# Kernel optimization log

Measured on AMD Instinct MI355X. Metric: run time of the kernel, lower is better.

## Reference

```python
import jax, jax.numpy as jnp
import numpy as np

N_NODES = 100000


def gcn_conv(x, edge_index, W, b, n_nodes):
    # PyG GCNConv: x' = D^{-1/2} (A + I) D^{-1/2} (X W) + b
    xw = x @ W  # [N, out]
    # add self loops
    loops = jnp.arange(n_nodes, dtype=edge_index.dtype)
    row = jnp.concatenate([edge_index[0], loops])  # source
    col = jnp.concatenate([edge_index[1], loops])  # target (aggregation index)
    # symmetric degree normalization based on target degree (with self loops)
    deg = jax.ops.segment_sum(jnp.ones_like(col, dtype=xw.dtype), col,
                              num_segments=n_nodes)
    dinv = jnp.where(deg > 0, jax.lax.rsqrt(deg), 0.0)
    norm = dinv[row] * dinv[col]  # [E+N]
    msgs = norm[:, None] * xw[row]  # [E+N, out]
    out = jax.ops.segment_sum(msgs, col, num_segments=n_nodes)
    return out + b


def setup_inputs() -> dict:
    key = jax.random.key(0)
    k1, k2, k3, k4 = jax.random.split(key, 4)
    N, F_in, H, C, E = N_NODES, 128, 16, 10, 3200000
    x = jax.random.normal(k1, (N, F_in), dtype=jnp.float32)
    edge_index = jax.random.randint(k2, (2, E), 0, N, dtype=jnp.int64)
    W1 = jax.random.normal(k3, (F_in, H), dtype=jnp.float32) / np.sqrt(F_in)
    b1 = jnp.zeros((H,), dtype=jnp.float32)
    W2 = jax.random.normal(k4, (H, C), dtype=jnp.float32) / np.sqrt(H)
    b2 = jnp.zeros((C,), dtype=jnp.float32)
    return {"x": x, "edge_index": edge_index, "W1": W1, "b1": b1,
            "W2": W2, "b2": b2}


def reference(x, edge_index, W1, b1, W2, b2):
    n = x.shape[0]
    h = jax.nn.relu(gcn_conv(x, edge_index, W1, b1, n))
    # dropout is identity in eval mode
    logits = gcn_conv(h, edge_index, W2, b2, n)
    return jax.nn.log_softmax(logits, axis=1)
```

## Files before the change

kernel.cpp:

```cpp
#include <hip/hip_runtime.h>
#include <hip/hip_bf16.h>
#include <math.h>

#define F_IN 128
#define HID  16
#define NCLS 10
#define BS   256
#define CH   16384
#define KPL  4

typedef unsigned int uint;
typedef unsigned short ushort;
typedef __attribute__((ext_vector_type(8))) short short8v;
typedef __attribute__((ext_vector_type(4))) float f32x4;

static __device__ __forceinline__ short f2bf(float f) {
    __hip_bfloat16 h = __float2bfloat16(f);
    return *reinterpret_cast<short*>(&h);
}
static __device__ __forceinline__ float bflo(uint u) {
    union { uint x; float f; } c; c.x = u << 16; return c.f;
}
static __device__ __forceinline__ float bfhi(uint u) {
    union { uint x; float f; } c; c.x = u & 0xffff0000u; return c.f;
}
static __device__ __forceinline__ uint packbf(float f0, float f1) {
    return (uint)(ushort)f2bf(f0) | ((uint)(ushort)f2bf(f1) << 16);
}

__global__ __launch_bounds__(1024) void k_hist2(const int* __restrict__ col, int* __restrict__ hist,
                                                int E, int nbv, int nchunk) {
    extern __shared__ int h[];
    int t = threadIdx.x, k = blockIdx.x;
    for (int i = t; i < nbv; i += 1024) h[i] = 0;
    __syncthreads();
    int start = k * CH, end = min(start + CH, E);
    for (int i = start + t; i < end; i += 1024) atomicAdd(&h[col[i] >> 8], 1);
    __syncthreads();
    for (int i = t; i < nbv; i += 1024) hist[(size_t)i * nchunk + k] = h[i];
}

__global__ void k_cscan(int* __restrict__ hist, int* __restrict__ bcnt, int nchunk, int nbv) {
    int wave = threadIdx.x >> 6, lane = threadIdx.x & 63;
    int b = blockIdx.x * 4 + wave;
    if (b >= nbv) return;
    int* hb = hist + (size_t)b * nchunk;
    int vals[KPL];
    int ls = 0;
    #pragma unroll
    for (int i = 0; i < KPL; ++i) {
        int k = lane * KPL + i;
        vals[i] = (k < nchunk) ? hb[k] : 0;
        ls += vals[i];
    }
    int inc = ls;
    #pragma unroll
    for (int d = 1; d < 64; d <<= 1) {
        int v = __shfl_up(inc, d, 64);
        if (lane >= d) inc += v;
    }
    int run = inc - ls;
    #pragma unroll
    for (int i = 0; i < KPL; ++i) {
        int k = lane * KPL + i;
        if (k < nchunk) { hb[k] = run; run += vals[i]; }
    }
    if (lane == 63) bcnt[b] = inc;
}

__global__ void k_bscan(const int* __restrict__ bcnt, int* __restrict__ boff, int nbv, int E) {
    __shared__ int s[512];
    int t = threadIdx.x;
    int v = (t < nbv) ? bcnt[t] : 0;
    s[t] = v;
    __syncthreads();
    for (int ofs = 1; ofs < 512; ofs <<= 1) {
        int val = (t >= ofs) ? s[t - ofs] : 0;
        __syncthreads();
        if (t >= ofs) s[t] += val;
        __syncthreads();
    }
    if (t < nbv) boff[t] = s[t] - v;
    if (t == nbv) boff[t] = E;
}

__global__ __launch_bounds__(1024) void k_binW(const int* __restrict__ row, const int* __restrict__ col,
                                               const int* __restrict__ hist, const int* __restrict__ boff,
                                               uint* __restrict__ pairs, int E, int nbv, int nchunk) {
    extern __shared__ int lds[];
    int* gbase = lds;
    int* cur   = lds + nbv;
    int t = threadIdx.x, k = blockIdx.x;
    for (int i = t; i < nbv; i += 1024) {
        gbase[i] = boff[i] + hist[(size_t)i * nchunk + k];
        cur[i] = 0;
    }
    __syncthreads();
    int start = k * CH, end = min(start + CH, E);
    for (int i = start + t; i < end; i += 1024) {
        int c = col[i];
        int b = c >> 8;
        int rk = atomicAdd(&cur[b], 1);
        pairs[gbase[b] + rk] = ((uint)row[i] << 8) | (uint)(c & (BS - 1));
    }
}

__global__ __launch_bounds__(1024) void k_nsp(const uint* __restrict__ pairs,
                                              const int* __restrict__ boff,
                                              int* __restrict__ off, float* __restrict__ dinv,
                                              int* __restrict__ srow, int N, int nbv, int E) {
    __shared__ int c[BS];
    __shared__ int s[BS];
    int b = blockIdx.x, t = threadIdx.x;
    if (t < BS) c[t] = 0;
    __syncthreads();
    int st = boff[b], en = boff[b + 1];
    for (int i = st + t; i < en; i += 1024) atomicAdd(&c[pairs[i] & (BS - 1)], 1);
    __syncthreads();
    int v = 0;
    if (t < BS) { v = c[t]; s[t] = v; }
    __syncthreads();
    for (int ofs = 1; ofs < BS; ofs <<= 1) {
        int val = 0;
        if (t < BS && t >= ofs) val = s[t - ofs];
        __syncthreads();
        if (t < BS && t >= ofs) s[t] += val;
        __syncthreads();
    }
    int mybase = 0;
    if (t < BS) {
        mybase = st + s[t] - v;
        int n = (b << 8) + t;
        if (n < N) {
            off[n] = mybase;
            dinv[n] = rsqrtf((float)v + 1.0f);
        }
    }
    if (b == nbv - 1 && t == 0) off[N] = E;
    __syncthreads();
    if (t < BS) { c[t] = mybase; s[t] = 0; }
    __syncthreads();
    for (int i = st + t; i < en; i += 1024) {
        uint pv = pairs[i];
        int cl = pv & (BS - 1);
        int p = c[cl] + atomicAdd(&s[cl], 1);
        srow[p] = (int)(pv >> 8);
    }
}

__global__ void k_xwm(const float* __restrict__ x, const float* __restrict__ W1,
                      const float* __restrict__ dinv, __hip_bfloat16* __restrict__ xws, int N) {
    int w = threadIdx.x >> 6, l = threadIdx.x & 63;
    int n0 = (blockIdx.x * 4 + w) * 16;
    if (n0 >= N) return;
    int h = l & 15;
    int kb8 = (l >> 4) << 3;
    short8v bfrag[4];
    #pragma unroll
    for (int kk = 0; kk < 4; ++kk) {
        #pragma unroll
        for (int j = 0; j < 8; ++j) {
            int k = kk * 32 + kb8 + j;
            bfrag[kk][j] = f2bf(W1[k * HID + h]);
        }
    }
    int rrow = n0 + h;
    const float* xr = x + (size_t)rrow * F_IN + kb8;
    f32x4 acc = {0.f, 0.f, 0.f, 0.f};
    #pragma unroll
    for (int kk = 0; kk < 4; ++kk) {
        const float4* p = reinterpret_cast<const float4*>(xr + kk * 32);
        float4 lo = p[0], hi = p[1];
        short8v a;
        a[0] = f2bf(lo.x); a[1] = f2bf(lo.y); a[2] = f2bf(lo.z); a[3] = f2bf(lo.w);
        a[4] = f2bf(hi.x); a[5] = f2bf(hi.y); a[6] = f2bf(hi.z); a[7] = f2bf(hi.w);
        acc = __builtin_amdgcn_mfma_f32_16x16x32_bf16(a, bfrag[kk], acc, 0, 0, 0);
    }
    #pragma unroll
    for (int j = 0; j < 4; ++j) {
        int n = n0 + ((l >> 4) << 2) + j;
        xws[(size_t)n * HID + h] = __float2bfloat16(acc[j] * dinv[n]);
    }
}

__global__ void k_agg1(const uint* __restrict__ xws32, const int* __restrict__ off,
                       const int* __restrict__ srow, const float* __restrict__ dinv,
                       const float* __restrict__ b1, uint* __restrict__ hs32, int N) {
    int gid = blockIdx.x * blockDim.x + threadIdx.x;
    int n = gid >> 3;
    int p = threadIdx.x & 7;
    if (n >= N) return;
    int s = off[n], e = off[n + 1];
    uint v = xws32[(size_t)n * 8 + p];
    float a0 = bflo(v), b0 = bfhi(v);
    float a1 = 0.f, b1a = 0.f, a2 = 0.f, b2a = 0.f, a3 = 0.f, b3a = 0.f;
    int i = s;
    for (; i + 7 < e; i += 8) {
        int r0 = srow[i],     r1 = srow[i + 1], r2 = srow[i + 2], r3 = srow[i + 3];
        int r4 = srow[i + 4], r5 = srow[i + 5], r6 = srow[i + 6], r7 = srow[i + 7];
        uint v0 = xws32[(size_t)r0 * 8 + p], v1 = xws32[(size_t)r1 * 8 + p];
        uint v2 = xws32[(size_t)r2 * 8 + p], v3 = xws32[(size_t)r3 * 8 + p];
        uint v4 = xws32[(size_t)r4 * 8 + p], v5 = xws32[(size_t)r5 * 8 + p];
        uint v6 = xws32[(size_t)r6 * 8 + p], v7 = xws32[(size_t)r7 * 8 + p];
        a0 += bflo(v0); b0 += bfhi(v0);  a1 += bflo(v1); b1a += bfhi(v1);
        a2 += bflo(v2); b2a += bfhi(v2); a3 += bflo(v3); b3a += bfhi(v3);
        a0 += bflo(v4); b0 += bfhi(v4);  a1 += bflo(v5); b1a += bfhi(v5);
        a2 += bflo(v6); b2a += bfhi(v6); a3 += bflo(v7); b3a += bfhi(v7);
    }
    for (; i < e; ++i) {
        uint vv = xws32[(size_t)srow[i] * 8 + p];
        a0 += bflo(vv); b0 += bfhi(vv);
    }
    float sl = (a0 + a1) + (a2 + a3);
    float sh = (b0 + b1a) + (b2a + b3a);
    float d = dinv[n];
    float h0 = d * sl + b1[2 * p];
    float h1 = d * sh + b1[2 * p + 1];
    h0 = h0 > 0.f ? h0 : 0.f;
    h1 = h1 > 0.f ? h1 : 0.f;
    hs32[(size_t)n * 8 + p] = packbf(d * h0, d * h1);
}

__global__ void k_agg2(const uint* __restrict__ hs32, const int* __restrict__ off,
                       const int* __restrict__ srow, const float* __restrict__ dinv,
                       const float* __restrict__ W2, const float* __restrict__ b2,
                       float* __restrict__ out, int N) {
    __shared__ float gs[32][17];
    __shared__ float W2s[HID * NCLS];
    __shared__ float b2s[NCLS];
    int t = threadIdx.x;
    if (t < HID * NCLS) W2s[t] = W2[t];
    if (t < NCLS) b2s[t] = b2[t];
    int grp = t >> 3, p = t & 7;
    int n = blockIdx.x * 32 + grp;
    float g0 = 0.f, g1 = 0.f;
    if (n < N) {
        int s = off[n], e = off[n + 1];
        uint v = hs32[(size_t)n * 8 + p];
        float a0 = bflo(v), b0 = bfhi(v);
        float a1 = 0.f, b1a = 0.f, a2 = 0.f, b2a = 0.f, a3 = 0.f, b3a = 0.f;
        int i = s;
        for (; i + 7 < e; i += 8) {
            int r0 = srow[i],     r1 = srow[i + 1], r2 = srow[i + 2], r3 = srow[i + 3];
            int r4 = srow[i + 4], r5 = srow[i + 5], r6 = srow[i + 6], r7 = srow[i + 7];
            uint v0 = hs32[(size_t)r0 * 8 + p], v1 = hs32[(size_t)r1 * 8 + p];
            uint v2 = hs32[(size_t)r2 * 8 + p], v3 = hs32[(size_t)r3 * 8 + p];
            uint v4 = hs32[(size_t)r4 * 8 + p], v5 = hs32[(size_t)r5 * 8 + p];
            uint v6 = hs32[(size_t)r6 * 8 + p], v7 = hs32[(size_t)r7 * 8 + p];
            a0 += bflo(v0); b0 += bfhi(v0);  a1 += bflo(v1); b1a += bfhi(v1);
            a2 += bflo(v2); b2a += bfhi(v2); a3 += bflo(v3); b3a += bfhi(v3);
            a0 += bflo(v4); b0 += bfhi(v4);  a1 += bflo(v5); b1a += bfhi(v5);
            a2 += bflo(v6); b2a += bfhi(v6); a3 += bflo(v7); b3a += bfhi(v7);
        }
        for (; i < e; ++i) {
            uint vv = hs32[(size_t)srow[i] * 8 + p];
            a0 += bflo(vv); b0 += bfhi(vv);
        }
        float d = dinv[n];
        g0 = d * ((a0 + a1) + (a2 + a3));
        g1 = d * ((b0 + b1a) + (b2a + b3a));
    }
    gs[grp][2 * p]     = g0;
    gs[grp][2 * p + 1] = g1;
    __syncthreads();
    if (t < 32) {
        int n2 = blockIdx.x * 32 + t;
        if (n2 < N) {
            float v[NCLS];
            float m = -INFINITY;
            #pragma unroll
            for (int c = 0; c < NCLS; ++c) {
                float a = b2s[c];
                #pragma unroll
                for (int j = 0; j < HID; ++j) a += gs[t][j] * W2s[j * NCLS + c];
                v[c] = a;
                m = fmaxf(m, a);
            }
            float ssum = 0.f;
            #pragma unroll
            for (int c = 0; c < NCLS; ++c) ssum += __expf(v[c] - m);
            float lse = m + __logf(ssum);
            #pragma unroll
            for (int c = 0; c < NCLS; ++c) out[(size_t)n2 * NCLS + c] = v[c] - lse;
        }
    }
}

extern "C" void kernel_launch(void* const* d_in, const int* in_sizes, int n_in,
                              void* d_out, int out_size, void* d_ws, size_t ws_size,
                              hipStream_t stream) {
    const float* x  = (const float*)d_in[0];
    const int*   ei = (const int*)d_in[1];
    const float* W1 = (const float*)d_in[2];
    const float* b1 = (const float*)d_in[3];
    const float* W2 = (const float*)d_in[4];
    const float* b2 = (const float*)d_in[5];
    float* out = (float*)d_out;

    const int N = in_sizes[0] / F_IN;
    const int E = in_sizes[1] / 2;
    const int* row = ei;
    const int* col = ei + E;

    const int nbv = (N + BS - 1) / BS;
    const int nchunk = (E + CH - 1) / CH;

    char* ws = (char*)d_ws;
    auto alignup = [](size_t v) { return (v + 255) & ~(size_t)255; };
    size_t offb = 0;
    int*   hist = (int*)  (ws + offb); offb += alignup((size_t)nbv * nchunk * 4);
    int*   bcnt = (int*)  (ws + offb); offb += alignup((size_t)(nbv + 1) * 4);
    int*   boff = (int*)  (ws + offb); offb += alignup((size_t)(nbv + 1) * 4);
    int*   off  = (int*)  (ws + offb); offb += alignup((size_t)(N + 1) * 4);
    float* dinv = (float*)(ws + offb); offb += alignup((size_t)N * 4);
    uint*  pairs= (uint*) (ws + offb); offb += alignup((size_t)E * 4);
    int*   srow = (int*)  (ws + offb); offb += alignup((size_t)E * 4);
    uint*  xws  = (uint*) (ws + offb); offb += alignup((size_t)N * HID * 2);
    uint*  hs   = (uint*) (ws + offb); offb += alignup((size_t)N * HID * 2);
    (void)ws_size; (void)n_in; (void)out_size;

    size_t histB = (size_t)nbv * 4;
    const int nxb = ((N / 16) + 3) / 4;

    k_hist2<<<nchunk, 1024, histB,     stream>>>(col, hist, E, nbv, nchunk);
    k_cscan<<<(nbv + 3) / 4, 256, 0,   stream>>>(hist, bcnt, nchunk, nbv);
    k_bscan<<<1, 512, 0,               stream>>>(bcnt, boff, nbv, E);
    k_binW <<<nchunk, 1024, 2 * histB, stream>>>(row, col, hist, boff, pairs, E, nbv, nchunk);
    k_nsp  <<<nbv, 1024, 0,            stream>>>(pairs, boff, off, dinv, srow, N, nbv, E);
    k_xwm  <<<nxb, 256, 0,             stream>>>(x, W1, dinv, (__hip_bfloat16*)xws, N);
    k_agg1 <<<(N * 8 + 255) / 256, 256, 0, stream>>>(xws, off, srow, dinv, b1, hs, N);
    k_agg2 <<<(N * 8 + 255) / 256, 256, 0, stream>>>(hs, off, srow, dinv, W2, b2, out, N);
}
```

Measured before the change: 123.8 us.

## Vectorize edge loads, cache bucket pairs in LDS, widen aggregation gathers to 64-bit

The histogram and binning kernels now read col/row as int4, so each thread handles four edges per iteration. The node-sort kernel stores its bucket's pairs in a 40KB LDS buffer during the counting pass and reads them back in the scatter pass instead of reloading from global memory. Both aggregation kernels now use 4 threads per node, each gathering a 64-bit chunk of the bf16 features, which halves the number of gather instructions per edge. Per-thread work rises and fewer threads are launched, and the large LDS array may lower occupancy in k_nsp.

```diff
diff --git a/kernel.cpp b/kernel.cpp
--- a/kernel.cpp
+++ b/kernel.cpp
@@ -8,6 +8,7 @@
 #define BS   256
 #define CH   16384
 #define KPL  4
+#define LDSCAP 10240
 
 typedef unsigned int uint;
 typedef unsigned short ushort;
@@ -35,7 +36,16 @@
     for (int i = t; i < nbv; i += 1024) h[i] = 0;
     __syncthreads();
     int start = k * CH, end = min(start + CH, E);
-    for (int i = start + t; i < end; i += 1024) atomicAdd(&h[col[i] >> 8], 1);
+    int cnt4 = (end - start) >> 2;
+    const int4* col4 = (const int4*)(col + start);
+    for (int i = t; i < cnt4; i += 1024) {
+        int4 c4 = col4[i];
+        atomicAdd(&h[c4.x >> 8], 1);
+        atomicAdd(&h[c4.y >> 8], 1);
+        atomicAdd(&h[c4.z >> 8], 1);
+        atomicAdd(&h[c4.w >> 8], 1);
+    }
+    for (int i = start + (cnt4 << 2) + t; i < end; i += 1024) atomicAdd(&h[col[i] >> 8], 1);
     __syncthreads();
     for (int i = t; i < nbv; i += 1024) hist[(size_t)i * nchunk + k] = h[i];
 }
@@ -97,7 +107,23 @@
     }
     __syncthreads();
     int start = k * CH, end = min(start + CH, E);
-    for (int i = start + t; i < end; i += 1024) {
+    int cnt4 = (end - start) >> 2;
+    const int4* col4 = (const int4*)(col + start);
+    const int4* row4 = (const int4*)(row + start);
+    for (int i = t; i < cnt4; i += 1024) {
+        int4 c4 = col4[i];
+        int4 r4 = row4[i];
+        int b0 = c4.x >> 8, b1 = c4.y >> 8, b2 = c4.z >> 8, b3 = c4.w >> 8;
+        int k0 = atomicAdd(&cur[b0], 1);
+        int k1 = atomicAdd(&cur[b1], 1);
+        int k2 = atomicAdd(&cur[b2], 1);
+        int k3 = atomicAdd(&cur[b3], 1);
+        pairs[gbase[b0] + k0] = ((uint)r4.x << 8) | (uint)(c4.x & (BS - 1));
+        pairs[gbase[b1] + k1] = ((uint)r4.y << 8) | (uint)(c4.y & (BS - 1));
+        pairs[gbase[b2] + k2] = ((uint)r4.z << 8) | (uint)(c4.z & (BS - 1));
+        pairs[gbase[b3] + k3] = ((uint)r4.w << 8) | (uint)(c4.w & (BS - 1));
+    }
+    for (int i = start + (cnt4 << 2) + t; i < end; i += 1024) {
         int c = col[i];
         int b = c >> 8;
         int rk = atomicAdd(&cur[b], 1);
@@ -111,11 +137,16 @@
                                               int* __restrict__ srow, int N, int nbv, int E) {
     __shared__ int c[BS];
     __shared__ int s[BS];
+    __shared__ uint pc[LDSCAP];
     int b = blockIdx.x, t = threadIdx.x;
     if (t < BS) c[t] = 0;
     __syncthreads();
     int st = boff[b], en = boff[b + 1];
-    for (int i = st + t; i < en; i += 1024) atomicAdd(&c[pairs[i] & (BS - 1)], 1);
+    for (int i = st + t; i < en; i += 1024) {
+        uint pv = pairs[i];
+        if (i - st < LDSCAP) pc[i - st] = pv;
+        atomicAdd(&c[pv & (BS - 1)], 1);
+    }
     __syncthreads();
     int v = 0;
     if (t < BS) { v = c[t]; s[t] = v; }
@@ -141,7 +172,7 @@
     if (t < BS) { c[t] = mybase; s[t] = 0; }
     __syncthreads();
     for (int i = st + t; i < en; i += 1024) {
-        uint pv = pairs[i];
+        uint pv = (i - st < LDSCAP) ? pc[i - st] : pairs[i];
         int cl = pv & (BS - 1);
         int p = c[cl] + atomicAdd(&s[cl], 1);
         srow[p] = (int)(pv >> 8);
@@ -183,88 +214,102 @@
     }
 }
 
-__global__ void k_agg1(const uint* __restrict__ xws32, const int* __restrict__ off,
+__global__ void k_agg1(const uint2* __restrict__ xw64, const int* __restrict__ off,
                        const int* __restrict__ srow, const float* __restrict__ dinv,
-                       const float* __restrict__ b1, uint* __restrict__ hs32, int N) {
+                       const float* __restrict__ b1, uint2* __restrict__ hs64, int N) {
     int gid = blockIdx.x * blockDim.x + threadIdx.x;
-    int n = gid >> 3;
-    int p = threadIdx.x & 7;
+    int n = gid >> 2;
+    int p = threadIdx.x & 3;
     if (n >= N) return;
     int s = off[n], e = off[n + 1];
-    uint v = xws32[(size_t)n * 8 + p];
-    float a0 = bflo(v), b0 = bfhi(v);
-    float a1 = 0.f, b1a = 0.f, a2 = 0.f, b2a = 0.f, a3 = 0.f, b3a = 0.f;
+    uint2 v = xw64[(size_t)n * 4 + p];
+    float a0 = bflo(v.x), a1 = bfhi(v.x), a2 = bflo(v.y), a3 = bfhi(v.y);
+    float c0 = 0.f, c1 = 0.f, c2 = 0.f, c3 = 0.f;
     int i = s;
     for (; i + 7 < e; i += 8) {
         int r0 = srow[i],     r1 = srow[i + 1], r2 = srow[i + 2], r3 = srow[i + 3];
         int r4 = srow[i + 4], r5 = srow[i + 5], r6 = srow[i + 6], r7 = srow[i + 7];
-        uint v0 = xws32[(size_t)r0 * 8 + p], v1 = xws32[(size_t)r1 * 8 + p];
-        uint v2 = xws32[(size_t)r2 * 8 + p], v3 = xws32[(size_t)r3 * 8 + p];
-        uint v4 = xws32[(size_t)r4 * 8 + p], v5 = xws32[(size_t)r5 * 8 + p];
-        uint v6 = xws32[(size_t)r6 * 8 + p], v7 = xws32[(size_t)r7 * 8 + p];
-        a0 += bflo(v0); b0 += bfhi(v0);  a1 += bflo(v1); b1a += bfhi(v1);
-        a2 += bflo(v2); b2a += bfhi(v2); a3 += bflo(v3); b3a += bfhi(v3);
-        a0 += bflo(v4); b0 += bfhi(v4);  a1 += bflo(v5); b1a += bfhi(v5);
-        a2 += bflo(v6); b2a += bfhi(v6); a3 += bflo(v7); b3a += bfhi(v7);
+        uint2 v0 = xw64[(size_t)r0 * 4 + p], v1 = xw64[(size_t)r1 * 4 + p];
+        uint2 v2 = xw64[(size_t)r2 * 4 + p], v3 = xw64[(size_t)r3 * 4 + p];
+        uint2 v4 = xw64[(size_t)r4 * 4 + p], v5 = xw64[(size_t)r5 * 4 + p];
+        uint2 v6 = xw64[(size_t)r6 * 4 + p], v7 = xw64[(size_t)r7 * 4 + p];
+        a0 += bflo(v0.x); a1 += bfhi(v0.x); a2 += bflo(v0.y); a3 += bfhi(v0.y);
+        c0 += bflo(v1.x); c1 += bfhi(v1.x); c2 += bflo(v1.y); c3 += bfhi(v1.y);
+        a0 += bflo(v2.x); a1 += bfhi(v2.x); a2 += bflo(v2.y); a3 += bfhi(v2.y);
+        c0 += bflo(v3.x); c1 += bfhi(v3.x); c2 += bflo(v3.y); c3 += bfhi(v3.y);
+        a0 += bflo(v4.x); a1 += bfhi(v4.x); a2 += bflo(v4.y); a3 += bfhi(v4.y);
+        c0 += bflo(v5.x); c1 += bfhi(v5.x); c2 += bflo(v5.y); c3 += bfhi(v5.y);
+        a0 += bflo(v6.x); a1 += bfhi(v6.x); a2 += bflo(v6.y); a3 += bfhi(v6.y);
+        c0 += bflo(v7.x); c1 += bfhi(v7.x); c2 += bflo(v7.y); c3 += bfhi(v7.y);
     }
     for (; i < e; ++i) {
-        uint vv = xws32[(size_t)srow[i] * 8 + p];
-        a0 += bflo(vv); b0 += bfhi(vv);
-    }
-    float sl = (a0 + a1) + (a2 + a3);
-    float sh = (b0 + b1a) + (b2a + b3a);
+        uint2 vv = xw64[(size_t)srow[i] * 4 + p];
+        a0 += bflo(vv.x); a1 += bfhi(vv.x); a2 += bflo(vv.y); a3 += bfhi(vv.y);
+    }
     float d = dinv[n];
-    float h0 = d * sl + b1[2 * p];
-    float h1 = d * sh + b1[2 * p + 1];
+    float h0 = d * (a0 + c0) + b1[4 * p + 0];
+    float h1 = d * (a1 + c1) + b1[4 * p + 1];
+    float h2 = d * (a2 + c2) + b1[4 * p + 2];
+    float h3 = d * (a3 + c3) + b1[4 * p + 3];
     h0 = h0 > 0.f ? h0 : 0.f;
     h1 = h1 > 0.f ? h1 : 0.f;
-    hs32[(size_t)n * 8 + p] = packbf(d * h0, d * h1);
-}
-
-__global__ void k_agg2(const uint* __restrict__ hs32, const int* __restrict__ off,
+    h2 = h2 > 0.f ? h2 : 0.f;
+    h3 = h3 > 0.f ? h3 : 0.f;
+    uint2 o;
+    o.x = packbf(d * h0, d * h1);
+    o.y = packbf(d * h2, d * h3);
+    hs64[(size_t)n * 4 + p] = o;
+}
+
+__global__ void k_agg2(const uint2* __restrict__ hs64, const int* __restrict__ off,
                        const int* __restrict__ srow, const float* __restrict__ dinv,
                        const float* __restrict__ W2, const float* __restrict__ b2,
                        float* __restrict__ out, int N) {
-    __shared__ float gs[32][17];
+    __shared__ float gs[64][17];
     __shared__ float W2s[HID * NCLS];
     __shared__ float b2s[NCLS];
     int t = threadIdx.x;
     if (t < HID * NCLS) W2s[t] = W2[t];
     if (t < NCLS) b2s[t] = b2[t];
-    int grp = t >> 3, p = t & 7;
-    int n = blockIdx.x * 32 + grp;
-    float g0 = 0.f, g1 = 0.f;
+    int grp = t >> 2, p = t & 3;
+    int n = blockIdx.x * 64 + grp;
+    float g0 = 0.f, g1 = 0.f, g2 = 0.f, g3 = 0.f;
     if (n < N) {
         int s = off[n], e = off[n + 1];
-        uint v = hs32[(size_t)n * 8 + p];
-        float a0 = bflo(v), b0 = bfhi(v);
-        float a1 = 0.f, b1a = 0.f, a2 = 0.f, b2a = 0.f, a3 = 0.f, b3a = 0.f;
+        uint2 v = hs64[(size_t)n * 4 + p];
+        float a0 = bflo(v.x), a1 = bfhi(v.x), a2 = bflo(v.y), a3 = bfhi(v.y);
+        float c0 = 0.f, c1 = 0.f, c2 = 0.f, c3 = 0.f;
         int i = s;
         for (; i + 7 < e; i += 8) {
             int r0 = srow[i],     r1 = srow[i + 1], r2 = srow[i + 2], r3 = srow[i + 3];
             int r4 = srow[i + 4], r5 = srow[i + 5], r6 = srow[i + 6], r7 = srow[i + 7];
-            uint v0 = hs32[(size_t)r0 * 8 + p], v1 = hs32[(size_t)r1 * 8 + p];
-            uint v2 = hs32[(size_t)r2 * 8 + p], v3 = hs32[(size_t)r3 * 8 + p];
-            uint v4 = hs32[(size_t)r4 * 8 + p], v5 = hs32[(size_t)r5 * 8 + p];
-            uint v6 = hs32[(size_t)r6 * 8 + p], v7 = hs32[(size_t)r7 * 8 + p];
-            a0 += bflo(v0); b0 += bfhi(v0);  a1 += bflo(v1); b1a += bfhi(v1);
-            a2 += bflo(v2); b2a += bfhi(v2); a3 += bflo(v3); b3a += bfhi(v3);
-            a0 += bflo(v4); b0 += bfhi(v4);  a1 += bflo(v5); b1a += bfhi(v5);
-            a2 += bflo(v6); b2a += bfhi(v6); a3 += bflo(v7); b3a += bfhi(v7);
+            uint2 v0 = hs64[(size_t)r0 * 4 + p], v1 = hs64[(size_t)r1 * 4 + p];
+            uint2 v2 = hs64[(size_t)r2 * 4 + p], v3 = hs64[(size_t)r3 * 4 + p];
+            uint2 v4 = hs64[(size_t)r4 * 4 + p], v5 = hs64[(size_t)r5 * 4 + p];
+            uint2 v6 = hs64[(size_t)r6 * 4 + p], v7 = hs64[(size_t)r7 * 4 + p];
+            a0 += bflo(v0.x); a1 += bfhi(v0.x); a2 += bflo(v0.y); a3 += bfhi(v0.y);
+            c0 += bflo(v1.x); c1 += bfhi(v1.x); c2 += bflo(v1.y); c3 += bfhi(v1.y);
+            a0 += bflo(v2.x); a1 += bfhi(v2.x); a2 += bflo(v2.y); a3 += bfhi(v2.y);
+            c0 += bflo(v3.x); c1 += bfhi(v3.x); c2 += bflo(v3.y); c3 += bfhi(v3.y);
+            a0 += bflo(v4.x); a1 += bfhi(v4.x); a2 += bflo(v4.y); a3 += bfhi(v4.y);
+            c0 += bflo(v5.x); c1 += bfhi(v5.x); c2 += bflo(v5.y); c3 += bfhi(v5.y);
+            a0 += bflo(v6.x); a1 += bfhi(v6.x); a2 += bflo(v6.y); a3 += bfhi(v6.y);
+            c0 += bflo(v7.x); c1 += bfhi(v7.x); c2 += bflo(v7.y); c3 += bfhi(v7.y);
         }
         for (; i < e; ++i) {
-            uint vv = hs32[(size_t)srow[i] * 8 + p];
-            a0 += bflo(vv); b0 += bfhi(vv);
+            uint2 vv = hs64[(size_t)srow[i] * 4 + p];
+            a0 += bflo(vv.x); a1 += bfhi(vv.x); a2 += bflo(vv.y); a3 += bfhi(vv.y);
         }
         float d = dinv[n];
-        g0 = d * ((a0 + a1) + (a2 + a3));
-        g1 = d * ((b0 + b1a) + (b2a + b3a));
-    }
-    gs[grp][2 * p]     = g0;
-    gs[grp][2 * p + 1] = g1;
-    __syncthreads();
-    if (t < 32) {
-        int n2 = blockIdx.x * 32 + t;
+        g0 = d * (a0 + c0); g1 = d * (a1 + c1); g2 = d * (a2 + c2); g3 = d * (a3 + c3);
+    }
+    gs[grp][4 * p + 0] = g0;
+    gs[grp][4 * p + 1] = g1;
+    gs[grp][4 * p + 2] = g2;
+    gs[grp][4 * p + 3] = g3;
+    __syncthreads();
+    if (t < 64) {
+        int n2 = blockIdx.x * 64 + t;
         if (n2 < N) {
             float v[NCLS];
             float m = -INFINITY;
@@ -315,8 +360,8 @@
     float* dinv = (float*)(ws + offb); offb += alignup((size_t)N * 4);
     uint*  pairs= (uint*) (ws + offb); offb += alignup((size_t)E * 4);
     int*   srow = (int*)  (ws + offb); offb += alignup((size_t)E * 4);
-    uint*  xws  = (uint*) (ws + offb); offb += alignup((size_t)N * HID * 2);
-    uint*  hs   = (uint*) (ws + offb); offb += alignup((size_t)N * HID * 2);
+    uint2* xws  = (uint2*)(ws + offb); offb += alignup((size_t)N * HID * 2);
+    uint2* hs   = (uint2*)(ws + offb); offb += alignup((size_t)N * HID * 2);
     (void)ws_size; (void)n_in; (void)out_size;
 
     size_t histB = (size_t)nbv * 4;
@@ -328,6 +373,6 @@
     k_binW <<<nchunk, 1024, 2 * histB, stream>>>(row, col, hist, boff, pairs, E, nbv, nchunk);
     k_nsp  <<<nbv, 1024, 0,            stream>>>(pairs, boff, off, dinv, srow, N, nbv, E);
     k_xwm  <<<nxb, 256, 0,             stream>>>(x, W1, dinv, (__hip_bfloat16*)xws, N);
-    k_agg1 <<<(N * 8 + 255) / 256, 256, 0, stream>>>(xws, off, srow, dinv, b1, hs, N);
-    k_agg2 <<<(N * 8 + 255) / 256, 256, 0, stream>>>(hs, off, srow, dinv, W2, b2, out, N);
-}
+    k_agg1 <<<(N * 4 + 255) / 256, 256, 0, stream>>>(xws, off, srow, dinv, b1, hs, N);
+    k_agg2 <<<(N * 4 + 255) / 256, 256, 0, stream>>>(hs, off, srow, dinv, W2, b2, out, N);
+}
```

After: 125.2 us. About the same (+1.2%).
